# Kernel tuning notes

Hardware: AMD Instinct MI355X
Metric: run time of the kernel (lower is better)

The kernel has to match this reference:

```python
import jax, jax.numpy as jnp
import numpy as np

B, CIN, F, L = 16, 4, 64, 4096
H = CIN * F   # d_model = 256
N = 32        # SSM state size (S4D)

def setup_inputs() -> dict:
    key = jax.random.key(0)
    ks = jax.random.split(key, 9)
    inp = jax.random.normal(ks[0], (B, CIN, F, L), dtype=jnp.float32)
    # S4D parameterization: dt log-uniform in [1e-3, 1e-1], A = -exp(log_A_real) + i*A_imag (S4D-Lin init)
    log_dt = jnp.log(10.0 ** jax.random.uniform(ks[1], (H,), minval=-3.0, maxval=-1.0)).astype(jnp.float32)
    log_A_real = jnp.log(0.5 * jnp.ones((H, N), dtype=jnp.float32))
    A_imag = jnp.broadcast_to(np.pi * jnp.arange(N, dtype=jnp.float32), (H, N)).copy()
    C_real = jax.random.normal(ks[2], (H, N), dtype=jnp.float32) * (0.5 ** 0.5)
    C_imag = jax.random.normal(ks[3], (H, N), dtype=jnp.float32) * (0.5 ** 0.5)
    D = jax.random.normal(ks[4], (H,), dtype=jnp.float32)
    W_out = jax.random.normal(ks[5], (H, H), dtype=jnp.float32) / jnp.sqrt(H).astype(jnp.float32)
    b_out = jnp.zeros((H,), dtype=jnp.float32)
    return {"inp": inp, "log_dt": log_dt, "log_A_real": log_A_real, "A_imag": A_imag,
            "C_real": C_real, "C_imag": C_imag, "D": D, "W_out": W_out, "b_out": b_out}

def _s4d_kernel(log_dt, log_A_real, A_imag, C_real, C_imag, length):
    dt = jnp.exp(log_dt)                              # (H,)
    A = -jnp.exp(log_A_real) + 1j * A_imag            # (H,N) complex
    dtA = A * dt[:, None]                             # (H,N)
    C = C_real + 1j * C_imag                          # (H,N)
    Ct = C * (jnp.exp(dtA) - 1.0) / A                 # ZOH discretization of B*C
    l = jnp.arange(length, dtype=jnp.float32)
    vand = jnp.exp(dtA[:, :, None] * l)               # (H,N,L) Vandermonde of exp(dt*A)
    return 2.0 * jnp.einsum('hn,hnl->hl', Ct, vand).real  # (H,L) float

def reference(inp, log_dt, log_A_real, A_imag, C_real, C_imag, D, W_out, b_out):
    b, cin, f, l = inp.shape
    # transpose(2,3) then transpose(1,2): (B,C,F,L) -> (B,L,C,F) -> reshape (B,L,H)
    x = jnp.transpose(inp, (0, 3, 1, 2)).reshape(b, l, cin * f)
    u = jnp.transpose(x, (0, 2, 1))                   # (B,H,L)
    K = _s4d_kernel(log_dt, log_A_real, A_imag, C_real, C_imag, l)  # (H,L)
    n = 2 * l
    y = jnp.fft.irfft(jnp.fft.rfft(u, n) * jnp.fft.rfft(K, n), n)[..., :l]  # causal conv
    y = y + D[:, None] * u                            # skip connection
    y = jnp.transpose(y, (0, 2, 1))                   # (B,L,H)
    y = jax.nn.gelu(y)                                # S4Block default activation
    y = y @ W_out.T + b_out                           # output linear, final_act='id'
    # transpose(1,2) then reshape: (B,L,H) -> (B,H,L) -> (B,C,F,L)
    return jnp.transpose(y, (0, 2, 1)).reshape(b, cin, f, l)
```

## Files before the change

kernel.cpp:

```cpp
#include <hip/hip_runtime.h>
#include <hip/hip_bf16.h>
#include <cstdint>

#define S4_H 256
#define S4_N 32
#define S4_L 4096
#define S4_B 16
#define S4_T 64
#define S4_C 64

typedef __attribute__((ext_vector_type(8))) short bf16x8;
typedef __attribute__((ext_vector_type(4))) float f32x4;

__device__ __forceinline__ uint32_t s4_f2bf(float f) {
    uint32_t u = __float_as_uint(f);
    return (u + 0x7fffu + ((u >> 16) & 1u)) >> 16;
}

__device__ __forceinline__ float s4_gelu(float x) {
    float x3 = x * x * x;
    float z = 1.5957691216057308f * fmaf(0.044715f, x3, x);
    float e = __expf(-z);
    return x / (1.0f + e);
}

__device__ __forceinline__ float s4_rowsum32(float v) {
    v += __int_as_float(__builtin_amdgcn_update_dpp(0, __float_as_int(v), 0x111, 0xf, 0xf, false));
    v += __int_as_float(__builtin_amdgcn_update_dpp(0, __float_as_int(v), 0x112, 0xf, 0xf, false));
    v += __int_as_float(__builtin_amdgcn_update_dpp(0, __float_as_int(v), 0x114, 0xf, 0xf, false));
    v += __int_as_float(__builtin_amdgcn_update_dpp(0, __float_as_int(v), 0x118, 0xf, 0xf, false));
    v += __int_as_float(__builtin_amdgcn_update_dpp(0, __float_as_int(v), 0x142, 0xf, 0xf, false));
    return v;
}

__global__ __launch_bounds__(64) void s4_tab_kernel(
        const float* __restrict__ log_dt, const float* __restrict__ log_A_real,
        const float* __restrict__ A_imag, const float* __restrict__ C_real,
        const float* __restrict__ C_imag,
        float* __restrict__ wT, ushort* __restrict__ Ebf,
        ushort* __restrict__ TMbf, ushort* __restrict__ Vbf) {
    const int h = blockIdx.x, tid = threadIdx.x, n = tid & 31;
    __shared__ float Ksh[S4_T];
    const int idx = h * 32 + n;
    float dt = expf(log_dt[h]);
    float Ar = -expf(log_A_real[idx]);
    float Ai = A_imag[idx];
    float er = expf(dt * Ar);
    float wr = er * cosf(dt * Ai);
    float wi = er * sinf(dt * Ai);
    float inv = 1.0f / (Ar * Ar + Ai * Ai);
    float mr = wr - 1.0f, mi = wi;
    float qr = (mr * Ar + mi * Ai) * inv;
    float qi = (mi * Ar - mr * Ai) * inv;
    float Cr = C_real[idx], Ci = C_imag[idx];
    float cr = 2.0f * (Cr * qr - Ci * qi);
    float ci = -2.0f * (Cr * qi + Ci * qr);
    ushort* Eh = Ebf + h * 4096;
    ushort* Vh = Vbf + h * 4096;
    float pr = 1.0f, pi = 0.0f;
    for (int t = 0; t < S4_T; ++t) {
        if (tid < 32) {
            Eh[(2 * n) * 64 + (63 - t)]     = (ushort)s4_f2bf(pr);
            Eh[(2 * n + 1) * 64 + (63 - t)] = (ushort)s4_f2bf(pi);
        }
        float kt = s4_rowsum32(fmaf(cr, pr, ci * pi));
        if (tid == 31) Ksh[t] = kt;
        float Qr = pr * wr - pi * wi;
        float Qi = pr * wi + pi * wr;
        if (tid < 32) {
            Vh[t * 64 + 2 * n]     = (ushort)s4_f2bf(fmaf(cr, Qr, ci * Qi));
            Vh[t * 64 + 2 * n + 1] = (ushort)s4_f2bf(fmaf(ci, Qr, -cr * Qi));
        }
        pr = Qr; pi = Qi;
    }
    if (tid < 32) { wT[idx] = pr; wT[8192 + idx] = pi; }
    __syncthreads();
    ushort* TMh = TMbf + h * 4096;
    for (int e = tid; e < 4096; e += 64) {
        int to = e >> 6, ti = e & 63;
        TMh[e] = (ti <= to) ? (ushort)s4_f2bf(Ksh[to - ti]) : (ushort)0;
    }
}

__global__ __launch_bounds__(256) void s4_wconv(const float* __restrict__ W,
                                               ushort* __restrict__ Wp) {
    const int m = threadIdx.x, ko = blockIdx.x;
    const float* src = W + (size_t)m * S4_H + ko * 8;
    float4 a = *(const float4*)src;
    float4 b = *(const float4*)(src + 4);
    uint4 pk;
    pk.x = s4_f2bf(a.x) | (s4_f2bf(a.y) << 16);
    pk.y = s4_f2bf(a.z) | (s4_f2bf(a.w) << 16);
    pk.z = s4_f2bf(b.x) | (s4_f2bf(b.y) << 16);
    pk.w = s4_f2bf(b.z) | (s4_f2bf(b.w) << 16);
    *(uint4*)(Wp + ((size_t)ko * S4_H + m) * 8) = pk;
}

__global__ __launch_bounds__(256, 6) void s4_scan_fused(
        const float* __restrict__ u, const float* __restrict__ wT,
        const ushort* __restrict__ Ebf, const ushort* __restrict__ TMbf,
        const ushort* __restrict__ Vbf, const float* __restrict__ D,
        uint32_t* __restrict__ g) {
    __shared__ char UXbfB[8192];
    __shared__ float Ssh[64][66];
    const int tid = threadIdx.x;
    const int bh = blockIdx.x;
    const int h = bh & (S4_H - 1);
    const int w = tid >> 6, lane = tid & 63;
    const int l15 = lane & 15, lg = lane >> 4;

    const float* up = u + (size_t)bh * S4_L;
    {
        const float4* uf = (const float4*)up;
        #pragma unroll
        for (int j = 0; j < 4; ++j) {
            int i = j * 256 + tid;
            float4 v = uf[i];
            uint2 pk;
            pk.x = s4_f2bf(v.x) | (s4_f2bf(v.y) << 16);
            pk.y = s4_f2bf(v.z) | (s4_f2bf(v.w) << 16);
            int o = i * 8;
            *(uint2*)(UXbfB + (o ^ (((o >> 7) & 7) << 4))) = pk;
        }
    }
    const int arow = 16 * w + l15;
    const size_t tb = (size_t)h * 4096 + (size_t)arow * 64 + lg * 8;
    bf16x8 eA0 = *(const bf16x8*)(Ebf + tb);
    bf16x8 eA1 = *(const bf16x8*)(Ebf + tb + 32);
    bf16x8 tA0 = *(const bf16x8*)(TMbf + tb);
    bf16x8 tA1 = *(const bf16x8*)(TMbf + tb + 32);
    bf16x8 vA0 = *(const bf16x8*)(Vbf + tb);
    bf16x8 vA1 = *(const bf16x8*)(Vbf + tb + 32);
    __syncthreads();

    bf16x8 ufr[4][2];
    uint2 eu[4];
    const int t0 = 16 * w + lg * 4;
    #pragma unroll
    for (int ct = 0; ct < 4; ++ct) {
        int c = ct * 16 + l15;
        int swz = (c & 7) << 4;
        ufr[ct][0] = *(const bf16x8*)(UXbfB + c * 128 + ((lg * 16) ^ swz));
        ufr[ct][1] = *(const bf16x8*)(UXbfB + c * 128 + ((64 + lg * 16) ^ swz));
        eu[ct] = *(const uint2*)(UXbfB + c * 128 + ((t0 * 2) ^ swz));
        f32x4 acc = {0.f, 0.f, 0.f, 0.f};
        acc = __builtin_amdgcn_mfma_f32_16x16x32_bf16(eA0, ufr[ct][0], acc, 0, 0, 0);
        acc = __builtin_amdgcn_mfma_f32_16x16x32_bf16(eA1, ufr[ct][1], acc, 0, 0, 0);
        *(f32x4*)(&Ssh[c][16 * w + lg * 4]) = acc;
    }
    __syncthreads();

    f32x4 yac[4];
    #pragma unroll
    for (int ct = 0; ct < 4; ++ct) {
        f32x4 y = {0.f, 0.f, 0.f, 0.f};
        y = __builtin_amdgcn_mfma_f32_16x16x32_bf16(tA0, ufr[ct][0], y, 0, 0, 0);
        if (w >= 2)
            y = __builtin_amdgcn_mfma_f32_16x16x32_bf16(tA1, ufr[ct][1], y, 0, 0, 0);
        yac[ct] = y;
    }

    if (tid < 32) {
        float wtr = wT[h * 32 + tid], wti = wT[8192 + h * 32 + tid];
        float xr = 0.f, xi = 0.f;
        #pragma unroll
        for (int c = 0; c < S4_C; ++c) {
            int o = c * 128 + tid * 4;
            *(uint32_t*)(UXbfB + (o ^ (((c & 7) << 4)))) = s4_f2bf(xr) | (s4_f2bf(xi) << 16);
            float2 s2 = *(const float2*)(&Ssh[c][2 * tid]);
            float nr2 = fmaf(wtr, xr, fmaf(-wti, xi, s2.x));
            float ni2 = fmaf(wtr, xi, fmaf(wti, xr, s2.y));
            xr = nr2; xi = ni2;
        }
    }
    __syncthreads();

    const float Dh = D[h];
    uint32_t* gp = g + (size_t)bh * (S4_L / 2);
    #pragma unroll
    for (int ct = 0; ct < 4; ++ct) {
        int c = ct * 16 + l15;
        int swz = (c & 7) << 4;
        bf16x8 xb0 = *(const bf16x8*)(UXbfB + c * 128 + ((lg * 16) ^ swz));
        bf16x8 xb1 = *(const bf16x8*)(UXbfB + c * 128 + ((64 + lg * 16) ^ swz));
        f32x4 y = yac[ct];
        y = __builtin_amdgcn_mfma_f32_16x16x32_bf16(vA0, xb0, y, 0, 0, 0);
        y = __builtin_amdgcn_mfma_f32_16x16x32_bf16(vA1, xb1, y, 0, 0, 0);
        uint2 upk = eu[ct];
        float u0 = __uint_as_float(upk.x << 16);
        float u1 = __uint_as_float(upk.x & 0xffff0000u);
        float u2 = __uint_as_float(upk.y << 16);
        float u3 = __uint_as_float(upk.y & 0xffff0000u);
        float g0 = s4_gelu(fmaf(Dh, u0, y[0]));
        float g1 = s4_gelu(fmaf(Dh, u1, y[1]));
        float g2 = s4_gelu(fmaf(Dh, u2, y[2]));
        float g3 = s4_gelu(fmaf(Dh, u3, y[3]));
        uint2 opk;
        opk.x = s4_f2bf(g0) | (s4_f2bf(g1) << 16);
        opk.y = s4_f2bf(g2) | (s4_f2bf(g3) << 16);
        *(uint2*)(gp + (c * 64 + t0) / 2) = opk;
    }
}

__global__ __launch_bounds__(256) void s4_g2p(const ushort* __restrict__ g,
                                              ushort* __restrict__ gP) {
    const int ho = blockIdx.x, b = blockIdx.y;
    const int t = threadIdx.x;
    const ushort* gbase = g + (size_t)(b * S4_H + ho * 8) * S4_L;
    ushort* pbase = gP + (size_t)(b * 32 + ho) * S4_L * 8;
    for (int it = 0; it < 8; ++it) {
        int l = it * 512 + t * 2;
        uint32_t r[8];
        #pragma unroll
        for (int i = 0; i < 8; ++i)
            r[i] = *(const uint32_t*)(gbase + (size_t)i * S4_L + l);
        uint4 lo, hi;
        lo.x = (r[0] & 0xffffu) | (r[1] << 16);
        lo.y = (r[2] & 0xffffu) | (r[3] << 16);
        lo.z = (r[4] & 0xffffu) | (r[5] << 16);
        lo.w = (r[6] & 0xffffu) | (r[7] << 16);
        hi.x = (r[0] >> 16) | (r[1] & 0xffff0000u);
        hi.y = (r[2] >> 16) | (r[3] & 0xffff0000u);
        hi.z = (r[4] >> 16) | (r[5] & 0xffff0000u);
        hi.w = (r[6] >> 16) | (r[7] & 0xffff0000u);
        *(uint4*)(pbase + (size_t)l * 8) = lo;
        *(uint4*)(pbase + (size_t)l * 8 + 8) = hi;
    }
}

__global__ __launch_bounds__(256) void s4_gemm_mfma(
        const ushort* __restrict__ gP, const ushort* __restrict__ Wp,
        const float* __restrict__ bias, float* __restrict__ out) {
    const int tid = threadIdx.x;
    const int wv = tid >> 6, lane = tid & 63;
    const int l15 = lane & 15, lg = lane >> 4;
    const int b = blockIdx.z;
    const int m0 = blockIdx.y << 6;
    const int l0 = ((blockIdx.x << 2) | wv) << 6;
    f32x4 acc[4][4] = {};
    const ushort* wpl = Wp + (size_t)(m0 + l15) * 8;
    const ushort* gpl = gP + ((size_t)(b * 32) * S4_L + l0 + l15) * 8;
    for (int kb = 0; kb < 8; ++kb) {
        const int ko = kb * 4 + lg;
        bf16x8 aF[4], bF[4];
        #pragma unroll
        for (int i = 0; i < 4; ++i)
            aF[i] = *(const bf16x8*)(wpl + ((size_t)ko * S4_H + i * 16) * 8);
        #pragma unroll
        for (int j = 0; j < 4; ++j)
            bF[j] = *(const bf16x8*)(gpl + ((size_t)ko * S4_L + j * 16) * 8);
        #pragma unroll
        for (int i = 0; i < 4; ++i)
            #pragma unroll
            for (int j = 0; j < 4; ++j)
                acc[i][j] = __builtin_amdgcn_mfma_f32_16x16x32_bf16(aF[i], bF[j], acc[i][j], 0, 0, 0);
    }
    float* ob = out + (size_t)b * S4_H * S4_L;
    #pragma unroll
    for (int i = 0; i < 4; ++i) {
        #pragma unroll
        for (int jj = 0; jj < 4; ++jj) {
            const int row = m0 + i * 16 + lg * 4 + jj;
            const float bv = bias[row];
            float* orow = ob + (size_t)row * S4_L + l0 + l15;
            #pragma unroll
            for (int j = 0; j < 4; ++j)
                orow[j * 16] = acc[i][j][jj] + bv;
        }
    }
}

extern "C" void kernel_launch(void* const* d_in, const int* in_sizes, int n_in,
                              void* d_out, int out_size, void* d_ws, size_t ws_size,
                              hipStream_t stream) {
    const float* inp        = (const float*)d_in[0];
    const float* log_dt     = (const float*)d_in[1];
    const float* log_A_real = (const float*)d_in[2];
    const float* A_imag     = (const float*)d_in[3];
    const float* C_real     = (const float*)d_in[4];
    const float* C_imag     = (const float*)d_in[5];
    const float* D          = (const float*)d_in[6];
    const float* W_out      = (const float*)d_in[7];
    const float* b_out      = (const float*)d_in[8];
    float* out = (float*)d_out;

    char* wsc = (char*)d_ws;
    size_t off = 0;
    float* wT     = (float*)(wsc + off);  off += (64 << 10);
    ushort* Ebf   = (ushort*)(wsc + off); off += (2 << 20);
    ushort* TMbf  = (ushort*)(wsc + off); off += (2 << 20);
    ushort* Vbf   = (ushort*)(wsc + off); off += (2 << 20);
    ushort* Wp    = (ushort*)(wsc + off); off += (128 << 10);
    uint32_t* g   = (uint32_t*)(wsc + off); off += (size_t)S4_B * S4_H * S4_L * 2;
    ushort* gP    = (ushort*)(wsc + off);

    hipLaunchKernelGGL(s4_tab_kernel, dim3(S4_H), dim3(64), 0, stream,
                       log_dt, log_A_real, A_imag, C_real, C_imag, wT, Ebf, TMbf, Vbf);
    hipLaunchKernelGGL(s4_wconv, dim3(32), dim3(256), 0, stream, W_out, Wp);
    hipLaunchKernelGGL(s4_scan_fused, dim3(S4_B * S4_H), dim3(256), 0, stream,
                       inp, wT, Ebf, TMbf, Vbf, D, g);
    hipLaunchKernelGGL(s4_g2p, dim3(32, S4_B), dim3(256), 0, stream,
                       (const ushort*)g, gP);
    hipLaunchKernelGGL(s4_gemm_mfma, dim3(S4_L / 256, S4_H / 64, S4_B), dim3(256), 0, stream,
                       gP, Wp, b_out, out);
}
```

Before: 82.60 us.

## Fuse bf16 repack of activations into GEMM via swizzled shared-memory staging

Removes the separate s4_g2p kernel that repacked the bf16 GELU output into a k-interleaved layout in global memory. Each GEMM block now loads a 256x64 tile of the activations, repacks it into an XOR-swizzled 32KB LDS buffer, and the four waves each compute a 64-row slice of the output against the full K from LDS. This saves one kernel launch and a full write and read of the repacked activation buffer. In exchange it uses more shared memory per block, and W is now read from global memory by every block.

```diff
diff --git a/kernel.cpp b/kernel.cpp
--- a/kernel.cpp
+++ b/kernel.cpp
@@ -202,44 +202,45 @@
     }
 }
 
-__global__ __launch_bounds__(256) void s4_g2p(const ushort* __restrict__ g,
-                                              ushort* __restrict__ gP) {
-    const int ho = blockIdx.x, b = blockIdx.y;
-    const int t = threadIdx.x;
-    const ushort* gbase = g + (size_t)(b * S4_H + ho * 8) * S4_L;
-    ushort* pbase = gP + (size_t)(b * 32 + ho) * S4_L * 8;
-    for (int it = 0; it < 8; ++it) {
-        int l = it * 512 + t * 2;
-        uint32_t r[8];
-        #pragma unroll
-        for (int i = 0; i < 8; ++i)
-            r[i] = *(const uint32_t*)(gbase + (size_t)i * S4_L + l);
-        uint4 lo, hi;
-        lo.x = (r[0] & 0xffffu) | (r[1] << 16);
-        lo.y = (r[2] & 0xffffu) | (r[3] << 16);
-        lo.z = (r[4] & 0xffffu) | (r[5] << 16);
-        lo.w = (r[6] & 0xffffu) | (r[7] << 16);
-        hi.x = (r[0] >> 16) | (r[1] & 0xffff0000u);
-        hi.y = (r[2] >> 16) | (r[3] & 0xffff0000u);
-        hi.z = (r[4] >> 16) | (r[5] & 0xffff0000u);
-        hi.w = (r[6] >> 16) | (r[7] & 0xffff0000u);
-        *(uint4*)(pbase + (size_t)l * 8) = lo;
-        *(uint4*)(pbase + (size_t)l * 8 + 8) = hi;
-    }
-}
-
 __global__ __launch_bounds__(256) void s4_gemm_mfma(
-        const ushort* __restrict__ gP, const ushort* __restrict__ Wp,
+        const ushort* __restrict__ g,
+        const ushort* __restrict__ Wp,
         const float* __restrict__ bias, float* __restrict__ out) {
+    __shared__ char GlB[32768];
     const int tid = threadIdx.x;
     const int wv = tid >> 6, lane = tid & 63;
     const int l15 = lane & 15, lg = lane >> 4;
-    const int b = blockIdx.z;
-    const int m0 = blockIdx.y << 6;
-    const int l0 = ((blockIdx.x << 2) | wv) << 6;
+    const int b = blockIdx.y;
+    const int l0 = blockIdx.x << 6;
+
+    {
+        const int ho = tid >> 3, lp = tid & 7;
+        const ushort* gb = g + ((size_t)(b * S4_H) + ho * 8) * S4_L + l0;
+        #pragma unroll
+        for (int it = 0; it < 4; ++it) {
+            const int ll = 2 * (lp + 8 * it);
+            uint32_t r[8];
+            #pragma unroll
+            for (int i = 0; i < 8; ++i)
+                r[i] = *(const uint32_t*)(gb + (size_t)i * S4_L + ll);
+            uint4 lo, hi;
+            lo.x = (r[0] & 0xffffu) | (r[1] << 16);
+            lo.y = (r[2] & 0xffffu) | (r[3] << 16);
+            lo.z = (r[4] & 0xffffu) | (r[5] << 16);
+            lo.w = (r[6] & 0xffffu) | (r[7] << 16);
+            hi.x = (r[0] >> 16) | (r[1] & 0xffff0000u);
+            hi.y = (r[2] >> 16) | (r[3] & 0xffff0000u);
+            hi.z = (r[4] >> 16) | (r[5] & 0xffff0000u);
+            hi.w = (r[6] >> 16) | (r[7] & 0xffff0000u);
+            *(uint4*)(GlB + ll * 512 + ((ho ^ (ll & 15)) << 4)) = lo;
+            *(uint4*)(GlB + (ll + 1) * 512 + ((ho ^ ((ll + 1) & 15)) << 4)) = hi;
+        }
+    }
+    __syncthreads();
+
     f32x4 acc[4][4] = {};
-    const ushort* wpl = Wp + (size_t)(m0 + l15) * 8;
-    const ushort* gpl = gP + ((size_t)(b * 32) * S4_L + l0 + l15) * 8;
+    const ushort* wpl = Wp + (size_t)(64 * wv + l15) * 8;
+    #pragma unroll
     for (int kb = 0; kb < 8; ++kb) {
         const int ko = kb * 4 + lg;
         bf16x8 aF[4], bF[4];
@@ -248,21 +249,22 @@
             aF[i] = *(const bf16x8*)(wpl + ((size_t)ko * S4_H + i * 16) * 8);
         #pragma unroll
         for (int j = 0; j < 4; ++j)
-            bF[j] = *(const bf16x8*)(gpl + ((size_t)ko * S4_L + j * 16) * 8);
+            bF[j] = *(const bf16x8*)(GlB + (j * 16 + l15) * 512 + ((ko ^ l15) << 4));
         #pragma unroll
         for (int i = 0; i < 4; ++i)
             #pragma unroll
             for (int j = 0; j < 4; ++j)
                 acc[i][j] = __builtin_amdgcn_mfma_f32_16x16x32_bf16(aF[i], bF[j], acc[i][j], 0, 0, 0);
     }
-    float* ob = out + (size_t)b * S4_H * S4_L;
+
+    float* ob = out + ((size_t)(b * S4_H) + 64 * wv) * S4_L + l0;
     #pragma unroll
     for (int i = 0; i < 4; ++i) {
         #pragma unroll
         for (int jj = 0; jj < 4; ++jj) {
-            const int row = m0 + i * 16 + lg * 4 + jj;
-            const float bv = bias[row];
-            float* orow = ob + (size_t)row * S4_L + l0 + l15;
+            const int mrow = i * 16 + lg * 4 + jj;
+            const float bv = bias[64 * wv + mrow];
+            float* orow = ob + (size_t)mrow * S4_L + l15;
             #pragma unroll
             for (int j = 0; j < 4; ++j)
                 orow[j * 16] = acc[i][j][jj] + bv;
@@ -291,16 +293,13 @@
     ushort* TMbf  = (ushort*)(wsc + off); off += (2 << 20);
     ushort* Vbf   = (ushort*)(wsc + off); off += (2 << 20);
     ushort* Wp    = (ushort*)(wsc + off); off += (128 << 10);
-    uint32_t* g   = (uint32_t*)(wsc + off); off += (size_t)S4_B * S4_H * S4_L * 2;
-    ushort* gP    = (ushort*)(wsc + off);
+    uint32_t* g   = (uint32_t*)(wsc + off);
 
     hipLaunchKernelGGL(s4_tab_kernel, dim3(S4_H), dim3(64), 0, stream,
                        log_dt, log_A_real, A_imag, C_real, C_imag, wT, Ebf, TMbf, Vbf);
     hipLaunchKernelGGL(s4_wconv, dim3(32), dim3(256), 0, stream, W_out, Wp);
     hipLaunchKernelGGL(s4_scan_fused, dim3(S4_B * S4_H), dim3(256), 0, stream,
                        inp, wT, Ebf, TMbf, Vbf, D, g);
-    hipLaunchKernelGGL(s4_g2p, dim3(32, S4_B), dim3(256), 0, stream,
-                       (const ushort*)g, gP);
-    hipLaunchKernelGGL(s4_gemm_mfma, dim3(S4_L / 256, S4_H / 64, S4_B), dim3(256), 0, stream,
-                       gP, Wp, b_out, out);
-}
+    hipLaunchKernelGGL(s4_gemm_mfma, dim3(S4_L / 64, S4_B), dim3(256), 0, stream,
+                       (const ushort*)g, Wp, b_out, out);
+}
```

Result: faster. 75.54 us (-8.5%).
